# Performance work log

Measured on AMD Instinct MI355X. Metric: run time of the kernel, lower is better.

The kernel has to match this reference:

```python
import jax, jax.numpy as jnp
import numpy as np

NEG_SLOPE = 0.2


def setup_inputs() -> dict:
    key = jax.random.key(0)
    k1, k2, k3, k4, k5 = jax.random.split(key, 5)
    N, F_in, F_out, H, D = 4096, 256, 256, 4, 64
    x = jax.random.normal(k1, (N, F_in), dtype=jnp.float32)
    adj = jax.random.normal(k2, (N, N), dtype=jnp.float32)  # ~half entries > 0 -> edges
    W = jax.random.normal(k3, (F_out, F_in), dtype=jnp.float32) * (1.0 / np.sqrt(F_in))
    a_src = jax.random.normal(k4, (H, D), dtype=jnp.float32) * 0.1
    a_dst = jax.random.normal(k5, (H, D), dtype=jnp.float32) * 0.1
    return {"x": x, "adj": adj, "W": W, "a_src": a_src, "a_dst": a_dst}


def reference(x, adj, W, a_src, a_dst):
    N = x.shape[0]
    H, D = a_src.shape
    # linear projection (torch Linear: x @ W.T), reshape to heads
    h = (x @ W.T).reshape(N, H, D)                      # [N, H, D]
    attn_src = jnp.einsum('nhd,hd->nh', h, a_src)       # [N, H]
    attn_dst = jnp.einsum('nhd,hd->nh', h, a_dst)       # [N, H]
    scores = attn_src[:, None, :] + attn_dst[None, :, :]  # [N, N, H]
    scores = jnp.where(scores >= 0, scores, NEG_SLOPE * scores)  # leaky_relu(0.2)
    mask = (adj > 0)[:, :, None]                        # [N, N, 1]
    scores = jnp.where(mask, scores, -jnp.inf)
    attn = jax.nn.softmax(scores, axis=1)               # softmax over neighbors j
    attn = jnp.nan_to_num(attn, nan=0.0)                # fully-masked rows -> 0
    weighted = attn * adj[:, :, None]                   # weight by adjacency values
    out = jnp.einsum('ijh,jhd->ihd', weighted, h)       # [N, H, D]
    return out.reshape(N, H * D)
```

## Files before the change

kernel.cpp:

```cpp
#include <hip/hip_runtime.h>
#include <stdint.h>

#define NN 4096
#define FF 256
#define HH 4
#define DD 64
#define NEG 0.2f
#define LOG2E 1.4426950408889634f

#define ITILE 32
#define NS 8
#define JR (NN / NS)
#define CJ 64
#define NCH (JR / CJ)
#define NB (NN / 8)

typedef __attribute__((ext_vector_type(8))) short short8;
typedef __attribute__((ext_vector_type(4))) float f32x4;
typedef __attribute__((ext_vector_type(16))) float f32x16;

__device__ __forceinline__ uint16_t bf16_rh(float f) {
    uint32_t u = __float_as_uint(f);
    return (uint16_t)((u + 0x8000u) >> 16);
}
__device__ __forceinline__ uint32_t pk2(float a, float b) {
    uint32_t ua = __float_as_uint(a) + 0x8000u;
    uint32_t ub = __float_as_uint(b) + 0x8000u;
    return (ua >> 16) | (ub & 0xffff0000u);
}
__device__ __forceinline__ short8 ld_bf8(const float* __restrict__ p) {
    float4 v0 = *(const float4*)p;
    float4 v1 = *(const float4*)(p + 4);
    union { uint32_t u[4]; short8 v; } o;
    o.u[0] = pk2(v0.x, v0.y); o.u[1] = pk2(v0.z, v0.w);
    o.u[2] = pk2(v1.x, v1.y); o.u[3] = pk2(v1.z, v1.w);
    return o.v;
}

__global__ __launch_bounds__(256) void gemm_h(const float* __restrict__ x,
                                              const float* __restrict__ W,
                                              const float* __restrict__ a_src,
                                              const float* __restrict__ a_dst,
                                              float* __restrict__ s,
                                              float* __restrict__ T_T,
                                              uint16_t* __restrict__ Bf,
                                              float* __restrict__ pden) {
    const int tid = threadIdx.x;
    if (blockIdx.y == 0) pden[blockIdx.x * 256 + tid] = 0.f;
    const int w = tid >> 6, l = tid & 63;
    const int m = l & 15, q = l >> 4;
    const int i0 = blockIdx.x * 64 + w * 16;
    const int f0 = blockIdx.y * 64;
    const int hh = blockIdx.y;
    f32x4 acc[4];
#pragma unroll
    for (int n = 0; n < 4; n++)
#pragma unroll
        for (int r = 0; r < 4; r++) acc[n][r] = 0.f;
    const float* arow = x + (size_t)(i0 + m) * FF + q * 8;
#pragma unroll
    for (int k0 = 0; k0 < FF; k0 += 32) {
        short8 af = ld_bf8(arow + k0);
#pragma unroll
        for (int n = 0; n < 4; n++) {
            short8 bf = ld_bf8(W + (size_t)(f0 + n * 16 + m) * FF + k0 + q * 8);
            acc[n] = __builtin_amdgcn_mfma_f32_16x16x32_bf16(af, bf, acc[n], 0, 0, 0);
        }
    }
    const float* as = a_src + hh * DD;
    const float* ad = a_dst + hh * DD;
    float av[4], dv[4];
#pragma unroll
    for (int n = 0; n < 4; n++) { av[n] = as[n * 16 + m]; dv[n] = ad[n * 16 + m]; }
#pragma unroll
    for (int r = 0; r < 4; r++) {
        float vs = 0.f, vd = 0.f;
#pragma unroll
        for (int n = 0; n < 4; n++) {
            vs = fmaf(acc[n][r], av[n], vs);
            vd = fmaf(acc[n][r], dv[n], vd);
        }
#pragma unroll
        for (int off = 1; off < 16; off <<= 1) {
            vs += __shfl_xor(vs, off, 64);
            vd += __shfl_xor(vd, off, 64);
        }
        if (m == 0) {
            const int i = i0 + q * 4 + r;
            s[(size_t)i * HH + hh] = vs * LOG2E;
            T_T[(size_t)hh * NN + i] = vd * LOG2E;
        }
    }
    const int iblk = blockIdx.x * 8 + w * 2 + (q >> 1);
    const int jjo  = (q & 1) * 4;
#pragma unroll
    for (int n = 0; n < 4; n++) {
        ushort4 o;
        o.x = bf16_rh(acc[n][0]); o.y = bf16_rh(acc[n][1]);
        o.z = bf16_rh(acc[n][2]); o.w = bf16_rh(acc[n][3]);
        *(ushort4*)(Bf + (((size_t)hh * NB + iblk) * 64 + n * 16 + m) * 8 + jjo) = o;
    }
}

__global__ __launch_bounds__(256, 4) void gat_main(
    const float* __restrict__ adj, const uint16_t* __restrict__ Bf,
    const float* __restrict__ s, const float* __restrict__ T_T,
    float* __restrict__ pden, uint16_t* __restrict__ part) {
    __shared__ float adj_s[2][CJ][ITILE + 1];
    const int tid = threadIdx.x;
    const int w = tid >> 6, l = tid & 63;
    const int m = l & 31, q = l >> 5;
    constexpr int NWG = (NN / ITILE) * NS;
    const int orig = blockIdx.y * (NN / ITILE) + blockIdx.x;
    const int swz = (orig & 7) * (NWG / 8) + (orig >> 3);
    const int i0 = (swz & (NN / ITILE - 1)) * ITILE;
    const int sl = swz / (NN / ITILE);
    const int jb = sl * JR;

    const float sS = s[(size_t)(i0 + m) * HH + w];
    const float sB = NEG * sS;
    float den = 0.f;
    f32x16 acc0, acc1;
#pragma unroll
    for (int r = 0; r < 16; r++) { acc0[r] = 0.f; acc1[r] = 0.f; }
    const float* trow = T_T + (size_t)w * NN;
    const uint16_t* bbase = Bf + (size_t)w * NB * 512;

    const int is = tid >> 3, j8 = (tid & 7) * 8;
    const float* arow = adj + (size_t)(i0 + is) * NN + j8;

    float4 p0 = *(const float4*)(arow + jb);
    float4 p1 = *(const float4*)(arow + jb + 4);
    adj_s[0][j8 + 0][is] = p0.x; adj_s[0][j8 + 1][is] = p0.y;
    adj_s[0][j8 + 2][is] = p0.z; adj_s[0][j8 + 3][is] = p0.w;
    adj_s[0][j8 + 4][is] = p1.x; adj_s[0][j8 + 5][is] = p1.y;
    adj_s[0][j8 + 6][is] = p1.z; adj_s[0][j8 + 7][is] = p1.w;
    p0 = *(const float4*)(arow + jb + CJ);
    p1 = *(const float4*)(arow + jb + CJ + 4);
    __syncthreads();

    for (int c = 0; c < NCH; ++c) {
        const int jc = jb + c * CJ;
        const int cur = c & 1;
        if (c + 1 < NCH) {
            const int nb = cur ^ 1;
            adj_s[nb][j8 + 0][is] = p0.x; adj_s[nb][j8 + 1][is] = p0.y;
            adj_s[nb][j8 + 2][is] = p0.z; adj_s[nb][j8 + 3][is] = p0.w;
            adj_s[nb][j8 + 4][is] = p1.x; adj_s[nb][j8 + 5][is] = p1.y;
            adj_s[nb][j8 + 6][is] = p1.z; adj_s[nb][j8 + 7][is] = p1.w;
            if (c + 2 < NCH) {
                p0 = *(const float4*)(arow + jc + 2 * CJ);
                p1 = *(const float4*)(arow + jc + 2 * CJ + 4);
            }
        }
#pragma unroll
        for (int kk = 0; kk < CJ; kk += 16) {
            const int jg = jc + kk + q * 8;
            const int jblk = ((jc + kk) >> 3) + q;
            float4 t0 = *(const float4*)(trow + jg);
            float4 t1 = *(const float4*)(trow + jg + 4);
            short8 bf0 = *(const short8*)(bbase + (size_t)jblk * 512 + m * 8);
            short8 bf1 = *(const short8*)(bbase + (size_t)jblk * 512 + (32 + m) * 8);
            float tt[8] = {t0.x, t0.y, t0.z, t0.w, t1.x, t1.y, t1.z, t1.w};
            uint32_t pk_[4];
#pragma unroll
            for (int jj = 0; jj < 8; jj += 2) {
                const int rr = kk + q * 8 + jj;
                float a0 = adj_s[cur][rr][m], a1 = adj_s[cur][rr + 1][m];
                float tv0 = tt[jj], tv1 = tt[jj + 1];
                float x0 = sS + tv0,           x1 = sS + tv1;
                float z0 = fmaf(NEG, tv0, sB), z1 = fmaf(NEG, tv1, sB);
                float lr0 = fmaxf(x0, z0), lr1 = fmaxf(x1, z1);
                float e0, e1;
                asm("v_exp_f32 %0, %1" : "=v"(e0) : "v"(lr0));
                asm("v_exp_f32 %0, %1" : "=v"(e1) : "v"(lr1));
                e0 = (a0 > 0.f) ? e0 : 0.f;
                e1 = (a1 > 0.f) ? e1 : 0.f;
                den += e0 + e1;
                pk_[jj >> 1] = pk2(e0 * a0, e1 * a1);
            }
            union { uint32_t u[4]; short8 v; } afu;
#pragma unroll
            for (int c4 = 0; c4 < 4; c4++) afu.u[c4] = pk_[c4];
            acc0 = __builtin_amdgcn_mfma_f32_32x32x16_bf16(afu.v, bf0, acc0, 0, 0, 0);
            acc1 = __builtin_amdgcn_mfma_f32_32x32x16_bf16(afu.v, bf1, acc1, 0, 0, 0);
        }
        __syncthreads();
    }
    den += __shfl_down(den, 32, 64);
    if (l < 32) atomicAdd(&pden[(size_t)(i0 + m) * HH + w], den);
    uint16_t* pbase = part + (size_t)sl * NN * FF;
#pragma unroll
    for (int reg = 0; reg < 16; reg++) {
        int row = (reg & 3) + 8 * (reg >> 2) + 4 * q;
        pbase[(size_t)(i0 + row) * FF + w * DD + m]      = bf16_rh(acc0[reg]);
        pbase[(size_t)(i0 + row) * FF + w * DD + 32 + m] = bf16_rh(acc1[reg]);
    }
}

__global__ __launch_bounds__(256) void finalize(const uint16_t* __restrict__ part,
                                                const float* __restrict__ pden,
                                                float* __restrict__ out) {
    const int i = blockIdx.x * 4 + (threadIdx.x >> 6);
    const int fq = (threadIdx.x & 63) * 4;
    float s0 = 0.f, s1 = 0.f, s2 = 0.f, s3 = 0.f;
#pragma unroll
    for (int sl = 0; sl < NS; sl++) {
        ushort4 v = *(const ushort4*)(part + (size_t)sl * NN * FF + (size_t)i * FF + fq);
        s0 += __uint_as_float(((uint32_t)v.x) << 16);
        s1 += __uint_as_float(((uint32_t)v.y) << 16);
        s2 += __uint_as_float(((uint32_t)v.z) << 16);
        s3 += __uint_as_float(((uint32_t)v.w) << 16);
    }
    float d = pden[(size_t)i * HH + (fq >> 6)];
    float inv = (d > 0.f) ? 1.f / d : 0.f;
    *(float4*)(out + (size_t)i * FF + fq) =
        make_float4(s0 * inv, s1 * inv, s2 * inv, s3 * inv);
}

extern "C" void kernel_launch(void* const* d_in, const int* in_sizes, int n_in,
                              void* d_out, int out_size, void* d_ws, size_t ws_size,
                              hipStream_t stream) {
    const float* x     = (const float*)d_in[0];
    const float* adj   = (const float*)d_in[1];
    const float* W     = (const float*)d_in[2];
    const float* a_src = (const float*)d_in[3];
    const float* a_dst = (const float*)d_in[4];
    float* out = (float*)d_out;

    char* ws = (char*)d_ws;
    uint16_t* Bf   = (uint16_t*)ws;
    float*    s    = (float*)(ws + (2u << 20));
    float*    T_T  = s + (size_t)NN * HH;
    float*    pden = T_T + (size_t)HH * NN;
    uint16_t* part = (uint16_t*)(ws + (3u << 20));

    gemm_h<<<dim3(NN / 64, HH), 256, 0, stream>>>(x, W, a_src, a_dst, s, T_T, Bf, pden);
    gat_main<<<dim3(NN / ITILE, NS), 256, 0, stream>>>(adj, Bf, s, T_T, pden, part);
    finalize<<<NN / 4, 256, 0, stream>>>(part, pden, out);
}
```

Before: 143.2 us.

## Stage GEMM operands in LDS, double adj chunk size, widen finalize loads

The projection GEMM now loads the x and W tiles once into shared memory as bf16 with coalesced float4 reads, instead of each wave re-reading and converting global rows per MFMA. The main attention kernel's adjacency chunk grows from 64 to 128 columns, with each thread prefetching 16 floats per chunk, which halves the number of barrier-separated iterations at the cost of more LDS and registers. The finalize kernel handles 8 features per thread with 16-byte loads and launches half as many blocks. The larger adj_s buffer, whose size depends on CJ, may reduce occupancy.

```diff
diff --git a/kernel.cpp b/kernel.cpp
--- a/kernel.cpp
+++ b/kernel.cpp
@@ -11,7 +11,7 @@
 #define ITILE 32
 #define NS 8
 #define JR (NN / NS)
-#define CJ 64
+#define CJ 128
 #define NCH (JR / CJ)
 #define NB (NN / 8)
 
@@ -28,13 +28,11 @@
     uint32_t ub = __float_as_uint(b) + 0x8000u;
     return (ua >> 16) | (ub & 0xffff0000u);
 }
-__device__ __forceinline__ short8 ld_bf8(const float* __restrict__ p) {
-    float4 v0 = *(const float4*)p;
-    float4 v1 = *(const float4*)(p + 4);
-    union { uint32_t u[4]; short8 v; } o;
-    o.u[0] = pk2(v0.x, v0.y); o.u[1] = pk2(v0.z, v0.w);
-    o.u[2] = pk2(v1.x, v1.y); o.u[3] = pk2(v1.z, v1.w);
-    return o.v;
+__device__ __forceinline__ ushort4 cvt_u4(float4 v) {
+    ushort4 o;
+    o.x = bf16_rh(v.x); o.y = bf16_rh(v.y);
+    o.z = bf16_rh(v.z); o.w = bf16_rh(v.w);
+    return o;
 }
 
 __global__ __launch_bounds__(256) void gemm_h(const float* __restrict__ x,
@@ -45,25 +43,41 @@
                                               float* __restrict__ T_T,
                                               uint16_t* __restrict__ Bf,
                                               float* __restrict__ pden) {
+    __shared__ uint16_t xs[64][264];
+    __shared__ uint16_t wsl[64][264];
     const int tid = threadIdx.x;
     if (blockIdx.y == 0) pden[blockIdx.x * 256 + tid] = 0.f;
+    const int i0g = blockIdx.x * 64;
+    const int f0 = blockIdx.y * 64;
+    const int hh = blockIdx.y;
+    const float* xsrc = x + (size_t)i0g * FF;
+    const float* wsrc = W + (size_t)f0 * FF;
+    {
+        const int rw = tid >> 6, c4 = (tid & 63) * 4;
+#pragma unroll
+        for (int p = 0; p < 16; p++) {
+            float4 vx = ((const float4*)xsrc)[p * 256 + tid];
+            float4 vw = ((const float4*)wsrc)[p * 256 + tid];
+            *(ushort4*)&xs[p * 4 + rw][c4] = cvt_u4(vx);
+            *(ushort4*)&wsl[p * 4 + rw][c4] = cvt_u4(vw);
+        }
+    }
+    __syncthreads();
     const int w = tid >> 6, l = tid & 63;
     const int m = l & 15, q = l >> 4;
-    const int i0 = blockIdx.x * 64 + w * 16;
-    const int f0 = blockIdx.y * 64;
-    const int hh = blockIdx.y;
+    const int i0 = i0g + w * 16;
     f32x4 acc[4];
 #pragma unroll
     for (int n = 0; n < 4; n++)
 #pragma unroll
         for (int r = 0; r < 4; r++) acc[n][r] = 0.f;
-    const float* arow = x + (size_t)(i0 + m) * FF + q * 8;
-#pragma unroll
-    for (int k0 = 0; k0 < FF; k0 += 32) {
-        short8 af = ld_bf8(arow + k0);
+    const uint16_t* ax = &xs[w * 16 + m][q * 8];
+#pragma unroll
+    for (int k0 = 0; k0 < 8; k0++) {
+        short8 af = *(const short8*)(ax + k0 * 32);
 #pragma unroll
         for (int n = 0; n < 4; n++) {
-            short8 bf = ld_bf8(W + (size_t)(f0 + n * 16 + m) * FF + k0 + q * 8);
+            short8 bf = *(const short8*)&wsl[n * 16 + m][k0 * 32 + q * 8];
             acc[n] = __builtin_amdgcn_mfma_f32_16x16x32_bf16(af, bf, acc[n], 0, 0, 0);
         }
     }
@@ -126,17 +140,21 @@
     const float* trow = T_T + (size_t)w * NN;
     const uint16_t* bbase = Bf + (size_t)w * NB * 512;
 
-    const int is = tid >> 3, j8 = (tid & 7) * 8;
-    const float* arow = adj + (size_t)(i0 + is) * NN + j8;
-
-    float4 p0 = *(const float4*)(arow + jb);
-    float4 p1 = *(const float4*)(arow + jb + 4);
-    adj_s[0][j8 + 0][is] = p0.x; adj_s[0][j8 + 1][is] = p0.y;
-    adj_s[0][j8 + 2][is] = p0.z; adj_s[0][j8 + 3][is] = p0.w;
-    adj_s[0][j8 + 4][is] = p1.x; adj_s[0][j8 + 5][is] = p1.y;
-    adj_s[0][j8 + 6][is] = p1.z; adj_s[0][j8 + 7][is] = p1.w;
-    p0 = *(const float4*)(arow + jb + CJ);
-    p1 = *(const float4*)(arow + jb + CJ + 4);
+    const int is = tid >> 3, j16 = (tid & 7) * 16;
+    const float* arow = adj + (size_t)(i0 + is) * NN + j16;
+
+    float4 pre[4];
+#pragma unroll
+    for (int c4 = 0; c4 < 4; c4++) pre[c4] = *(const float4*)(arow + jb + c4 * 4);
+#pragma unroll
+    for (int c4 = 0; c4 < 4; c4++) {
+        adj_s[0][j16 + c4 * 4 + 0][is] = pre[c4].x;
+        adj_s[0][j16 + c4 * 4 + 1][is] = pre[c4].y;
+        adj_s[0][j16 + c4 * 4 + 2][is] = pre[c4].z;
+        adj_s[0][j16 + c4 * 4 + 3][is] = pre[c4].w;
+    }
+#pragma unroll
+    for (int c4 = 0; c4 < 4; c4++) pre[c4] = *(const float4*)(arow + jb + CJ + c4 * 4);
     __syncthreads();
 
     for (int c = 0; c < NCH; ++c) {
@@ -144,13 +162,17 @@
         const int cur = c & 1;
         if (c + 1 < NCH) {
             const int nb = cur ^ 1;
-            adj_s[nb][j8 + 0][is] = p0.x; adj_s[nb][j8 + 1][is] = p0.y;
-            adj_s[nb][j8 + 2][is] = p0.z; adj_s[nb][j8 + 3][is] = p0.w;
-            adj_s[nb][j8 + 4][is] = p1.x; adj_s[nb][j8 + 5][is] = p1.y;
-            adj_s[nb][j8 + 6][is] = p1.z; adj_s[nb][j8 + 7][is] = p1.w;
+#pragma unroll
+            for (int c4 = 0; c4 < 4; c4++) {
+                adj_s[nb][j16 + c4 * 4 + 0][is] = pre[c4].x;
+                adj_s[nb][j16 + c4 * 4 + 1][is] = pre[c4].y;
+                adj_s[nb][j16 + c4 * 4 + 2][is] = pre[c4].z;
+                adj_s[nb][j16 + c4 * 4 + 3][is] = pre[c4].w;
+            }
             if (c + 2 < NCH) {
-                p0 = *(const float4*)(arow + jc + 2 * CJ);
-                p1 = *(const float4*)(arow + jc + 2 * CJ + 4);
+#pragma unroll
+                for (int c4 = 0; c4 < 4; c4++)
+                    pre[c4] = *(const float4*)(arow + jc + 2 * CJ + c4 * 4);
             }
         }
 #pragma unroll
@@ -201,21 +223,25 @@
 __global__ __launch_bounds__(256) void finalize(const uint16_t* __restrict__ part,
                                                 const float* __restrict__ pden,
                                                 float* __restrict__ out) {
-    const int i = blockIdx.x * 4 + (threadIdx.x >> 6);
-    const int fq = (threadIdx.x & 63) * 4;
-    float s0 = 0.f, s1 = 0.f, s2 = 0.f, s3 = 0.f;
+    const int i = blockIdx.x * 8 + (threadIdx.x >> 5);
+    const int f8 = (threadIdx.x & 31) * 8;
+    float acc[8];
+#pragma unroll
+    for (int e = 0; e < 8; e++) acc[e] = 0.f;
 #pragma unroll
     for (int sl = 0; sl < NS; sl++) {
-        ushort4 v = *(const ushort4*)(part + (size_t)sl * NN * FF + (size_t)i * FF + fq);
-        s0 += __uint_as_float(((uint32_t)v.x) << 16);
-        s1 += __uint_as_float(((uint32_t)v.y) << 16);
-        s2 += __uint_as_float(((uint32_t)v.z) << 16);
-        s3 += __uint_as_float(((uint32_t)v.w) << 16);
-    }
-    float d = pden[(size_t)i * HH + (fq >> 6)];
+        union { short8 v; uint16_t u[8]; } b;
+        b.v = *(const short8*)(part + (size_t)sl * NN * FF + (size_t)i * FF + f8);
+#pragma unroll
+        for (int e = 0; e < 8; e++)
+            acc[e] += __uint_as_float(((uint32_t)b.u[e]) << 16);
+    }
+    float d = pden[(size_t)i * HH + (f8 >> 6)];
     float inv = (d > 0.f) ? 1.f / d : 0.f;
-    *(float4*)(out + (size_t)i * FF + fq) =
-        make_float4(s0 * inv, s1 * inv, s2 * inv, s3 * inv);
+    *(float4*)(out + (size_t)i * FF + f8) =
+        make_float4(acc[0] * inv, acc[1] * inv, acc[2] * inv, acc[3] * inv);
+    *(float4*)(out + (size_t)i * FF + f8 + 4) =
+        make_float4(acc[4] * inv, acc[5] * inv, acc[6] * inv, acc[7] * inv);
 }
 
 extern "C" void kernel_launch(void* const* d_in, const int* in_sizes, int n_in,
@@ -237,5 +263,5 @@
 
     gemm_h<<<dim3(NN / 64, HH), 256, 0, stream>>>(x, W, a_src, a_dst, s, T_T, Bf, pden);
     gat_main<<<dim3(NN / ITILE, NS), 256, 0, stream>>>(adj, Bf, s, T_T, pden, part);
-    finalize<<<NN / 4, 256, 0, stream>>>(part, pden, out);
-}
+    finalize<<<NN / 8, 256, 0, stream>>>(part, pden, out);
+}
```

Result: faster. 134.7 us (-5.9%).
